# Kernel tuning notes

Measured on AMD Instinct MI355X. Metric: run time of the kernel, lower is better.

Reference implementation:

```python
import jax, jax.numpy as jnp
import numpy as np

B, T, D, H, O = 1024, 2048, 13, 128, 2


def setup_inputs() -> dict:
    key = jax.random.key(0)
    k1, k2, k3, k4 = jax.random.split(key, 4)
    xs = jax.random.normal(k1, (B, T, D), dtype=jnp.float32)
    # nn.Linear(in, out, bias=False) weights: [out, in]
    W_in = jax.random.normal(k2, (H, D), dtype=jnp.float32) / np.sqrt(D).astype(np.float32)
    W_h = jax.random.normal(k3, (H, H), dtype=jnp.float32) / np.sqrt(H).astype(np.float32)
    W_out = jax.random.normal(k4, (O, H), dtype=jnp.float32) / np.sqrt(H).astype(np.float32)
    return {"xs": xs, "W_in": W_in, "W_h": W_h, "W_out": W_out}


def reference(xs, W_in, W_h, W_out):
    # Vanilla hardtanh RNN, h0 = 0 (first step y = hardtanh(in_h(x)) == hardtanh(in_h(x) + W_h @ 0)).
    # Precompute all input projections in one big GEMM: [B, T, H]
    pre = jnp.einsum('btd,hd->bth', xs, W_in)

    def step(h, xh_t):  # h: [B, H], xh_t: [B, H]
        h = jnp.clip(xh_t + h @ W_h.T, -1.0, 1.0)  # F.hardtanh
        return h, None

    h0 = jnp.zeros((xs.shape[0], W_in.shape[0]), dtype=xs.dtype)
    hT, _ = jax.lax.scan(step, h0, jnp.swapaxes(pre, 0, 1))  # scan over time
    # Only the final hidden state per sequence is projected to the output.
    return hT @ W_out.T  # [B, O]
```

## Files before the change

### kernel.cpp

```cpp
#include <hip/hip_runtime.h>
#include <stdint.h>


#define RNN_B 1024
#define RNN_T 2048
#define RNN_D 13
#define RNN_H 128
#define RNN_O 2

#define NB 16
#define NWAVE 4
#define NTHR (NWAVE * 64)

using f32x4 = __attribute__((ext_vector_type(4))) float;
using v8s   = __attribute__((ext_vector_type(8))) short;

__device__ __forceinline__ short f2bf(float f) {
    union { float f; uint32_t u; } c; c.f = f;
    uint32_t u = c.u + 0x7fffu + ((c.u >> 16) & 1u);
    return (short)(u >> 16);
}
__device__ __forceinline__ float bf2fs(short s) {
    union { uint32_t u; float f; } c; c.u = ((uint32_t)(uint16_t)s) << 16;
    return c.f;
}
__device__ __forceinline__ float bitf(uint32_t u) {
    union { uint32_t u; float f; } c; c.u = u; return c.f;
}
__device__ __forceinline__ uint32_t cvtpk(float a, float b) {
    uint32_t r;
    asm("v_cvt_pk_bf16_f32 %0, %1, %2" : "=v"(r) : "v"(a), "v"(b));
    return r;
}
__device__ __forceinline__ v8s pack4(uint32_t a, uint32_t b, uint32_t c, uint32_t d) {
    union { uint32_t u[4]; v8s s; } z;
    z.u[0] = a; z.u[1] = b; z.u[2] = c; z.u[3] = d; return z.s;
}
__device__ __forceinline__ float clamp1(float v) {
    return __builtin_amdgcn_fmed3f(v, -1.0f, 1.0f);
}

__device__ __forceinline__ void barrier_lgkm() {
    __builtin_amdgcn_sched_barrier(0);
    asm volatile("s_waitcnt lgkmcnt(0)" ::: "memory");
    __builtin_amdgcn_s_barrier();
    asm volatile("" ::: "memory");
    __builtin_amdgcn_sched_barrier(0);
}

#define MFMA(a, b, c) __builtin_amdgcn_mfma_f32_16x16x32_bf16((a), (b), (c), 0, 0, 0)

#define STEP(CUR, NXT, X0, X1, X2, X3, TPF)                                      \
  do {                                                                           \
                     \
    v8s bh1 = *(const v8s*)&Hhi[CUR][off1];                                      \
    v8s bl1 = *(const v8s*)&Hlo[CUR][off1];                                      \
    v8s bh2 = *(const v8s*)&Hhi[CUR][off2];                                      \
    v8s bl2 = *(const v8s*)&Hlo[CUR][off2];                                      \
    v8s bh3 = *(const v8s*)&Hhi[CUR][off3];                                      \
    v8s bl3 = *(const v8s*)&Hlo[CUR][off3];                                      \
                                \
    float m0 = X0, m1 = X1, m2 = X2, m3 = X3;                                    \
    if (g == 3) { m1 = 0.0f; m2 = 0.0f; m3 = 0.0f; }                             \
    uint32_t xh01 = cvtpk(m0, m1), xh23 = cvtpk(m2, m3);                         \
    float q0 = m0 - bitf(xh01 << 16);                                            \
    float q1 = m1 - bitf(xh01 & 0xffff0000u);                                    \
    float q2 = m2 - bitf(xh23 << 16);                                            \
    float q3 = m3 - bitf(xh23 & 0xffff0000u);                                    \
    uint32_t xl01 = cvtpk(q0, q1), xl23 = cvtpk(q2, q3);                         \
    v8s xh = pack4(xh01, xh23, 0u, 0u);                                          \
    v8s xl = pack4(xl01, xl23, 0u, 0u);                                          \
                    \
    f32x4 Z = {0.f, 0.f, 0.f, 0.f};                                              \
    f32x4 A1 = MFMA(whiA[4], xh, Z);                                             \
    f32x4 A2 = MFMA(whiA[4], xl, Z);                                             \
    f32x4 A3 = MFMA(wloA[4], xh, Z);                                             \
    A1 = MFMA(whiA[0], selfBh, A1);                                              \
    A2 = MFMA(whiA[0], selfBl, A2);                                              \
    A3 = MFMA(wloA[0], selfBh, A3);                                              \
             \
    if ((TPF) < RNN_T) {                                                         \
      const float* xp = xrow + (size_t)(TPF) * RNN_D;                            \
      X0 = xp[d0]; X1 = xp[d1]; X2 = xp[d2]; X3 = xp[d3];                        \
    }                                                                            \
    A1 = MFMA(whiA[1], bh1, A1);                                                 \
    A2 = MFMA(whiA[1], bl1, A2);                                                 \
    A3 = MFMA(wloA[1], bh1, A3);                                                 \
    A1 = MFMA(whiA[2], bh2, A1);                                                 \
    A2 = MFMA(whiA[2], bl2, A2);                                                 \
    A3 = MFMA(wloA[2], bh2, A3);                                                 \
    A1 = MFMA(whiA[3], bh3, A1);                                                 \
    A2 = MFMA(whiA[3], bl3, A2);                                                 \
    A3 = MFMA(wloA[3], bh3, A3);                                                 \
                \
    f32x4 B1 = MFMA(whiB[4], xh, Z);                                             \
    f32x4 B2 = MFMA(whiB[4], xl, Z);                                             \
    f32x4 B3 = MFMA(wloB[4], xh, Z);                                             \
    B1 = MFMA(whiB[0], selfBh, B1);                                              \
    B2 = MFMA(whiB[0], selfBl, B2);                                              \
    B3 = MFMA(wloB[0], selfBh, B3);                                              \
    float v0 = clamp1(A1[0] + A2[0] + A3[0]);                                    \
    float v1 = clamp1(A1[1] + A2[1] + A3[1]);                                    \
    float v2 = clamp1(A1[2] + A2[2] + A3[2]);                                    \
    float v3 = clamp1(A1[3] + A2[3] + A3[3]);                                    \
    B1 = MFMA(whiB[1], bh1, B1);                                                 \
    B2 = MFMA(whiB[1], bl1, B2);                                                 \
    B3 = MFMA(wloB[1], bh1, B3);                                                 \
    uint32_t h01A = cvtpk(v0, v1), h23A = cvtpk(v2, v3);                         \
    float p0 = v0 - bitf(h01A << 16);                                            \
    float p1 = v1 - bitf(h01A & 0xffff0000u);                                    \
    float p2 = v2 - bitf(h23A << 16);                                            \
    float p3 = v3 - bitf(h23A & 0xffff0000u);                                    \
    B1 = MFMA(whiB[2], bh2, B1);                                                 \
    B2 = MFMA(whiB[2], bl2, B2);                                                 \
    B3 = MFMA(wloB[2], bh2, B3);                                                 \
    uint32_t l01A = cvtpk(p0, p1), l23A = cvtpk(p2, p3);                         \
    B1 = MFMA(whiB[3], bh3, B1);                                                 \
    B2 = MFMA(whiB[3], bl3, B2);                                                 \
    B3 = MFMA(wloB[3], bh3, B3);                                                 \
        \
    {                                                                            \
      float w0 = clamp1(B1[0] + B2[0] + B3[0]);                                  \
      float w1 = clamp1(B1[1] + B2[1] + B3[1]);                                  \
      float w2 = clamp1(B1[2] + B2[2] + B3[2]);                                  \
      float w3 = clamp1(B1[3] + B2[3] + B3[3]);                                  \
      uint32_t h01B = cvtpk(w0, w1), h23B = cvtpk(w2, w3);                       \
      float r0 = w0 - bitf(h01B << 16);                                          \
      float r1 = w1 - bitf(h01B & 0xffff0000u);                                  \
      float r2 = w2 - bitf(h23B << 16);                                          \
      float r3 = w3 - bitf(h23B & 0xffff0000u);                                  \
      uint32_t l01B = cvtpk(r0, r1), l23B = cvtpk(r2, r3);                       \
      selfBh = pack4(h01A, h23A, h01B, h23B);                                    \
      selfBl = pack4(l01A, l23A, l01B, l23B);                                    \
      *(v8s*)&Hhi[NXT][offw] = selfBh;                                           \
      *(v8s*)&Hlo[NXT][offw] = selfBl;                                           \
    }                                                                            \
    barrier_lgkm();                                                              \
  } while (0)

__global__ __launch_bounds__(NTHR, 1) void rnn_mfma18_kernel(
    const float* __restrict__ xs,
    const float* __restrict__ W_in,
    const float* __restrict__ W_h,
    const float* __restrict__ W_out,
    float* __restrict__ out)
{
    __shared__ __align__(16) short Hhi[2][NB * 128];
    __shared__ __align__(16) short Hlo[2][NB * 128];

    const int tid  = threadIdx.x;
    const int lane = tid & 63;
    const int wid  = tid >> 6;
    const int n    = lane & 15;
    const int g    = lane >> 4;
    const int b0   = blockIdx.x * NB;

    const int off1 = n * 128 + (((((wid + 1) & 3) << 2) + g) ^ n) * 8;
    const int off2 = n * 128 + (((((wid + 2) & 3) << 2) + g) ^ n) * 8;
    const int off3 = n * 128 + (((((wid + 3) & 3) << 2) + g) ^ n) * 8;
    const int offw = n * 128 + (((wid << 2) + g) ^ n) * 8;

    const int d0 = (4 * g + 0 > 12) ? 12 : 4 * g + 0;
    const int d1 = (4 * g + 1 > 12) ? 12 : 4 * g + 1;
    const int d2 = (4 * g + 2 > 12) ? 12 : 4 * g + 2;
    const int d3 = (4 * g + 3 > 12) ? 12 : 4 * g + 3;

    v8s whiA[5], wloA[5], whiB[5], wloB[5];
    #pragma unroll
    for (int mi = 0; mi < 2; ++mi) {
        const int row = 16 * (wid * 2 + mi) + n;
        #pragma unroll
        for (int q = 0; q < 4; ++q) {
            const int kt = (wid + q) & 3;
            v8s h8, l8;
            #pragma unroll
            for (int j = 0; j < 4; ++j) {
                const float w1 = W_h[row * RNN_H + 32 * kt + 4 * g + j];
                const float w2 = W_h[row * RNN_H + 32 * kt + 16 + 4 * g + j];
                const short h1 = f2bf(w1);
                const short h2 = f2bf(w2);
                h8[j] = h1; h8[4 + j] = h2;
                l8[j] = f2bf(w1 - bf2fs(h1));
                l8[4 + j] = f2bf(w2 - bf2fs(h2));
            }
            if (mi == 0) { whiA[q] = h8; wloA[q] = l8; }
            else         { whiB[q] = h8; wloB[q] = l8; }
        }
        {
            v8s h8, l8;
            #pragma unroll
            for (int j = 0; j < 4; ++j) {
                const int kx = 4 * g + j;
                const float w1 = (kx < RNN_D) ? W_in[row * RNN_D + kx] : 0.0f;
                const short h1 = f2bf(w1);
                h8[j] = h1; h8[4 + j] = 0;
                l8[j] = f2bf(w1 - bf2fs(h1));
                l8[4 + j] = 0;
            }
            if (mi == 0) { whiA[4] = h8; wloA[4] = l8; }
            else         { whiB[4] = h8; wloB[4] = l8; }
        }
    }

    for (int idx = tid; idx < NB * 128; idx += NTHR) {
        Hhi[0][idx] = 0;
        Hlo[0][idx] = 0;
    }

    v8s selfBh = {0, 0, 0, 0, 0, 0, 0, 0};
    v8s selfBl = {0, 0, 0, 0, 0, 0, 0, 0};

    const float* xrow = xs + (size_t)(b0 + n) * RNN_T * RNN_D;
    float xa0 = xrow[d0], xa1 = xrow[d1], xa2 = xrow[d2], xa3 = xrow[d3];
    float xb0 = xrow[RNN_D + d0], xb1 = xrow[RNN_D + d1];
    float xb2 = xrow[RNN_D + d2], xb3 = xrow[RNN_D + d3];
    __syncthreads();

    for (int t = 0; t < RNN_T; t += 2) {
        STEP(0, 1, xa0, xa1, xa2, xa3, t + 2);
        STEP(1, 0, xb0, xb1, xb2, xb3, t + 3);
    }

    __syncthreads();

    if (wid == 0 && lane < NB * RNN_O) {
        const int nn = lane & 15;
        const int o  = lane >> 4;
        float acc = 0.0f;
        for (int i = 0; i < RNN_H; ++i) {
            const int pos = 32 * (i >> 5) + 8 * ((i >> 2) & 3)
                          + 4 * ((i >> 4) & 1) + (i & 3);
            const int adr = nn * 128 + ((pos >> 3) ^ nn) * 8 + (pos & 7);
            const float hv = bf2fs(Hhi[0][adr]) + bf2fs(Hlo[0][adr]);
            acc = fmaf(W_out[o * RNN_H + i], hv, acc);
        }
        out[(size_t)(b0 + nn) * RNN_O + o] = acc;
    }
}

extern "C" void kernel_launch(void* const* d_in, const int* in_sizes, int n_in,
                              void* d_out, int out_size, void* d_ws, size_t ws_size,
                              hipStream_t stream) {
    const float* xs    = (const float*)d_in[0];
    const float* W_in  = (const float*)d_in[1];
    const float* W_h   = (const float*)d_in[2];
    const float* W_out = (const float*)d_in[3];
    float* out = (float*)d_out;

    rnn_mfma18_kernel<<<RNN_B / NB, NTHR, 0, stream>>>(xs, W_in, W_h, W_out, out);
}
```

Measured before the change: 1.217 ms.

## Ping-pong two batch groups per block to overlap MFMA phase with epilogue

Each block now handles 32 sequences as two independent 16-sequence groups of four waves, each with its own double-buffered hidden-state LDS. The recurrent step is split into an MFMA phase and a clamp/convert/store phase, and the groups run out of phase: one group does its matrix multiplies while the other does its epilogue, separated by block barriers. The MFMA chains for the two output tiles are also interleaved, so independent accumulators hide MFMA latency. The cost is twice as many barriers per time step, shared across 8 waves, and half as many blocks.

```diff
diff --git a/kernel.cpp b/kernel.cpp
--- a/kernel.cpp
+++ b/kernel.cpp
@@ -8,9 +8,10 @@
 #define RNN_H 128
 #define RNN_O 2
 
-#define NB 16
-#define NWAVE 4
-#define NTHR (NWAVE * 64)
+#define NBPG 16
+#define NB   32
+#define NBLK (RNN_B / NB)
+#define NTHR 512
 
 using f32x4 = __attribute__((ext_vector_type(4))) float;
 using v8s   = __attribute__((ext_vector_type(8))) short;
@@ -50,16 +51,14 @@
 
 #define MFMA(a, b, c) __builtin_amdgcn_mfma_f32_16x16x32_bf16((a), (b), (c), 0, 0, 0)
 
-#define STEP(CUR, NXT, X0, X1, X2, X3, TPF)                                      \
+#define S1(BUFR, X0, X1, X2, X3, TPF)                                            \
   do {                                                                           \
-                     \
-    v8s bh1 = *(const v8s*)&Hhi[CUR][off1];                                      \
-    v8s bl1 = *(const v8s*)&Hlo[CUR][off1];                                      \
-    v8s bh2 = *(const v8s*)&Hhi[CUR][off2];                                      \
-    v8s bl2 = *(const v8s*)&Hlo[CUR][off2];                                      \
-    v8s bh3 = *(const v8s*)&Hhi[CUR][off3];                                      \
-    v8s bl3 = *(const v8s*)&Hlo[CUR][off3];                                      \
-                                \
+    v8s bh1 = *(const v8s*)&Hh[BUFR][off1];                                      \
+    v8s bl1 = *(const v8s*)&Hl[BUFR][off1];                                      \
+    v8s bh2 = *(const v8s*)&Hh[BUFR][off2];                                      \
+    v8s bl2 = *(const v8s*)&Hl[BUFR][off2];                                      \
+    v8s bh3 = *(const v8s*)&Hh[BUFR][off3];                                      \
+    v8s bl3 = *(const v8s*)&Hl[BUFR][off3];                                      \
     float m0 = X0, m1 = X1, m2 = X2, m3 = X3;                                    \
     if (g == 3) { m1 = 0.0f; m2 = 0.0f; m3 = 0.0f; }                             \
     uint32_t xh01 = cvtpk(m0, m1), xh23 = cvtpk(m2, m3);                         \
@@ -70,95 +69,97 @@
     uint32_t xl01 = cvtpk(q0, q1), xl23 = cvtpk(q2, q3);                         \
     v8s xh = pack4(xh01, xh23, 0u, 0u);                                          \
     v8s xl = pack4(xl01, xl23, 0u, 0u);                                          \
-                    \
     f32x4 Z = {0.f, 0.f, 0.f, 0.f};                                              \
-    f32x4 A1 = MFMA(whiA[4], xh, Z);                                             \
-    f32x4 A2 = MFMA(whiA[4], xl, Z);                                             \
-    f32x4 A3 = MFMA(wloA[4], xh, Z);                                             \
-    A1 = MFMA(whiA[0], selfBh, A1);                                              \
-    A2 = MFMA(whiA[0], selfBl, A2);                                              \
-    A3 = MFMA(wloA[0], selfBh, A3);                                              \
-             \
+    P1 = MFMA(whiA[4], xh, Z);                                                   \
+    Q1 = MFMA(whiB[4], xh, Z);                                                   \
+    P2 = MFMA(whiA[4], xl, Z);                                                   \
+    Q2 = MFMA(whiB[4], xl, Z);                                                   \
+    P3 = MFMA(wloA[4], xh, Z);                                                   \
+    Q3 = MFMA(wloB[4], xh, Z);                                                   \
+    P1 = MFMA(whiA[0], selfBh, P1);                                              \
+    Q1 = MFMA(whiB[0], selfBh, Q1);                                              \
+    P2 = MFMA(whiA[0], selfBl, P2);                                              \
+    Q2 = MFMA(whiB[0], selfBl, Q2);                                              \
+    P3 = MFMA(wloA[0], selfBh, P3);                                              \
+    Q3 = MFMA(wloB[0], selfBh, Q3);                                              \
     if ((TPF) < RNN_T) {                                                         \
       const float* xp = xrow + (size_t)(TPF) * RNN_D;                            \
       X0 = xp[d0]; X1 = xp[d1]; X2 = xp[d2]; X3 = xp[d3];                        \
     }                                                                            \
-    A1 = MFMA(whiA[1], bh1, A1);                                                 \
-    A2 = MFMA(whiA[1], bl1, A2);                                                 \
-    A3 = MFMA(wloA[1], bh1, A3);                                                 \
-    A1 = MFMA(whiA[2], bh2, A1);                                                 \
-    A2 = MFMA(whiA[2], bl2, A2);                                                 \
-    A3 = MFMA(wloA[2], bh2, A3);                                                 \
-    A1 = MFMA(whiA[3], bh3, A1);                                                 \
-    A2 = MFMA(whiA[3], bl3, A2);                                                 \
-    A3 = MFMA(wloA[3], bh3, A3);                                                 \
-                \
-    f32x4 B1 = MFMA(whiB[4], xh, Z);                                             \
-    f32x4 B2 = MFMA(whiB[4], xl, Z);                                             \
-    f32x4 B3 = MFMA(wloB[4], xh, Z);                                             \
-    B1 = MFMA(whiB[0], selfBh, B1);                                              \
-    B2 = MFMA(whiB[0], selfBl, B2);                                              \
-    B3 = MFMA(wloB[0], selfBh, B3);                                              \
-    float v0 = clamp1(A1[0] + A2[0] + A3[0]);                                    \
-    float v1 = clamp1(A1[1] + A2[1] + A3[1]);                                    \
-    float v2 = clamp1(A1[2] + A2[2] + A3[2]);                                    \
-    float v3 = clamp1(A1[3] + A2[3] + A3[3]);                                    \
-    B1 = MFMA(whiB[1], bh1, B1);                                                 \
-    B2 = MFMA(whiB[1], bl1, B2);                                                 \
-    B3 = MFMA(wloB[1], bh1, B3);                                                 \
+    P1 = MFMA(whiA[1], bh1, P1);                                                 \
+    Q1 = MFMA(whiB[1], bh1, Q1);                                                 \
+    P2 = MFMA(whiA[1], bl1, P2);                                                 \
+    Q2 = MFMA(whiB[1], bl1, Q2);                                                 \
+    P3 = MFMA(wloA[1], bh1, P3);                                                 \
+    Q3 = MFMA(wloB[1], bh1, Q3);                                                 \
+    P1 = MFMA(whiA[2], bh2, P1);                                                 \
+    Q1 = MFMA(whiB[2], bh2, Q1);                                                 \
+    P2 = MFMA(whiA[2], bl2, P2);                                                 \
+    Q2 = MFMA(whiB[2], bl2, Q2);                                                 \
+    P3 = MFMA(wloA[2], bh2, P3);                                                 \
+    Q3 = MFMA(wloB[2], bh2, Q3);                                                 \
+    P1 = MFMA(whiA[3], bh3, P1);                                                 \
+    Q1 = MFMA(whiB[3], bh3, Q1);                                                 \
+    P2 = MFMA(whiA[3], bl3, P2);                                                 \
+    Q2 = MFMA(whiB[3], bl3, Q2);                                                 \
+    P3 = MFMA(wloA[3], bh3, P3);                                                 \
+    Q3 = MFMA(wloB[3], bh3, Q3);                                                 \
+  } while (0)
+
+#define S2(BUFW)                                                                 \
+  do {                                                                           \
+    float v0 = clamp1(P1[0] + P2[0] + P3[0]);                                    \
+    float v1 = clamp1(P1[1] + P2[1] + P3[1]);                                    \
+    float v2 = clamp1(P1[2] + P2[2] + P3[2]);                                    \
+    float v3 = clamp1(P1[3] + P2[3] + P3[3]);                                    \
     uint32_t h01A = cvtpk(v0, v1), h23A = cvtpk(v2, v3);                         \
     float p0 = v0 - bitf(h01A << 16);                                            \
     float p1 = v1 - bitf(h01A & 0xffff0000u);                                    \
     float p2 = v2 - bitf(h23A << 16);                                            \
     float p3 = v3 - bitf(h23A & 0xffff0000u);                                    \
-    B1 = MFMA(whiB[2], bh2, B1);                                                 \
-    B2 = MFMA(whiB[2], bl2, B2);                                                 \
-    B3 = MFMA(wloB[2], bh2, B3);                                                 \
     uint32_t l01A = cvtpk(p0, p1), l23A = cvtpk(p2, p3);                         \
-    B1 = MFMA(whiB[3], bh3, B1);                                                 \
-    B2 = MFMA(whiB[3], bl3, B2);                                                 \
-    B3 = MFMA(wloB[3], bh3, B3);                                                 \
-        \
-    {                                                                            \
-      float w0 = clamp1(B1[0] + B2[0] + B3[0]);                                  \
-      float w1 = clamp1(B1[1] + B2[1] + B3[1]);                                  \
-      float w2 = clamp1(B1[2] + B2[2] + B3[2]);                                  \
-      float w3 = clamp1(B1[3] + B2[3] + B3[3]);                                  \
-      uint32_t h01B = cvtpk(w0, w1), h23B = cvtpk(w2, w3);                       \
-      float r0 = w0 - bitf(h01B << 16);                                          \
-      float r1 = w1 - bitf(h01B & 0xffff0000u);                                  \
-      float r2 = w2 - bitf(h23B << 16);                                          \
-      float r3 = w3 - bitf(h23B & 0xffff0000u);                                  \
-      uint32_t l01B = cvtpk(r0, r1), l23B = cvtpk(r2, r3);                       \
-      selfBh = pack4(h01A, h23A, h01B, h23B);                                    \
-      selfBl = pack4(l01A, l23A, l01B, l23B);                                    \
-      *(v8s*)&Hhi[NXT][offw] = selfBh;                                           \
-      *(v8s*)&Hlo[NXT][offw] = selfBl;                                           \
-    }                                                                            \
-    barrier_lgkm();                                                              \
+    float w0 = clamp1(Q1[0] + Q2[0] + Q3[0]);                                    \
+    float w1 = clamp1(Q1[1] + Q2[1] + Q3[1]);                                    \
+    float w2 = clamp1(Q1[2] + Q2[2] + Q3[2]);                                    \
+    float w3 = clamp1(Q1[3] + Q2[3] + Q3[3]);                                    \
+    uint32_t h01B = cvtpk(w0, w1), h23B = cvtpk(w2, w3);                         \
+    float r0 = w0 - bitf(h01B << 16);                                            \
+    float r1 = w1 - bitf(h01B & 0xffff0000u);                                    \
+    float r2 = w2 - bitf(h23B << 16);                                            \
+    float r3 = w3 - bitf(h23B & 0xffff0000u);                                    \
+    uint32_t l01B = cvtpk(r0, r1), l23B = cvtpk(r2, r3);                         \
+    selfBh = pack4(h01A, h23A, h01B, h23B);                                      \
+    selfBl = pack4(l01A, l23A, l01B, l23B);                                      \
+    *(v8s*)&Hh[BUFW][offw] = selfBh;                                             \
+    *(v8s*)&Hl[BUFW][offw] = selfBl;                                             \
   } while (0)
 
-__global__ __launch_bounds__(NTHR, 1) void rnn_mfma18_kernel(
+__global__ __launch_bounds__(NTHR, 1) void rnn_mfma20_kernel(
     const float* __restrict__ xs,
     const float* __restrict__ W_in,
     const float* __restrict__ W_h,
     const float* __restrict__ W_out,
     float* __restrict__ out)
 {
-    __shared__ __align__(16) short Hhi[2][NB * 128];
-    __shared__ __align__(16) short Hlo[2][NB * 128];
+    __shared__ __align__(16) short Hhi[2][2][NBPG * 128];
+    __shared__ __align__(16) short Hlo[2][2][NBPG * 128];
 
     const int tid  = threadIdx.x;
     const int lane = tid & 63;
     const int wid  = tid >> 6;
+    const int grp  = __builtin_amdgcn_readfirstlane(wid >> 2);
+    const int wg   = wid & 3;
     const int n    = lane & 15;
     const int g    = lane >> 4;
-    const int b0   = blockIdx.x * NB;
-
-    const int off1 = n * 128 + (((((wid + 1) & 3) << 2) + g) ^ n) * 8;
-    const int off2 = n * 128 + (((((wid + 2) & 3) << 2) + g) ^ n) * 8;
-    const int off3 = n * 128 + (((((wid + 3) & 3) << 2) + g) ^ n) * 8;
-    const int offw = n * 128 + (((wid << 2) + g) ^ n) * 8;
+    const int b0   = blockIdx.x * NB + grp * NBPG;
+
+    short (*Hh)[NBPG * 128] = Hhi[grp];
+    short (*Hl)[NBPG * 128] = Hlo[grp];
+
+    const int off1 = n * 128 + (((((wg + 1) & 3) << 2) + g) ^ n) * 8;
+    const int off2 = n * 128 + (((((wg + 2) & 3) << 2) + g) ^ n) * 8;
+    const int off3 = n * 128 + (((((wg + 3) & 3) << 2) + g) ^ n) * 8;
+    const int offw = n * 128 + (((wg << 2) + g) ^ n) * 8;
 
     const int d0 = (4 * g + 0 > 12) ? 12 : 4 * g + 0;
     const int d1 = (4 * g + 1 > 12) ? 12 : 4 * g + 1;
@@ -168,10 +169,10 @@
     v8s whiA[5], wloA[5], whiB[5], wloB[5];
     #pragma unroll
     for (int mi = 0; mi < 2; ++mi) {
-        const int row = 16 * (wid * 2 + mi) + n;
+        const int row = 16 * (wg * 2 + mi) + n;
         #pragma unroll
         for (int q = 0; q < 4; ++q) {
-            const int kt = (wid + q) & 3;
+            const int kt = (wg + q) & 3;
             v8s h8, l8;
             #pragma unroll
             for (int j = 0; j < 4; ++j) {
@@ -202,13 +203,15 @@
         }
     }
 
-    for (int idx = tid; idx < NB * 128; idx += NTHR) {
-        Hhi[0][idx] = 0;
-        Hlo[0][idx] = 0;
+    for (int idx = tid; idx < 2 * 2 * NBPG * 128; idx += NTHR) {
+        (&Hhi[0][0][0])[idx] = 0;
+        (&Hlo[0][0][0])[idx] = 0;
     }
 
     v8s selfBh = {0, 0, 0, 0, 0, 0, 0, 0};
     v8s selfBl = {0, 0, 0, 0, 0, 0, 0, 0};
+    f32x4 P1 = {0.f, 0.f, 0.f, 0.f};
+    f32x4 P2 = P1, P3 = P1, Q1 = P1, Q2 = P1, Q3 = P1;
 
     const float* xrow = xs + (size_t)(b0 + n) * RNN_T * RNN_D;
     float xa0 = xrow[d0], xa1 = xrow[d1], xa2 = xrow[d2], xa3 = xrow[d3];
@@ -216,14 +219,25 @@
     float xb2 = xrow[RNN_D + d2], xb3 = xrow[RNN_D + d3];
     __syncthreads();
 
-    for (int t = 0; t < RNN_T; t += 2) {
-        STEP(0, 1, xa0, xa1, xa2, xa3, t + 2);
-        STEP(1, 0, xb0, xb1, xb2, xb3, t + 3);
-    }
-
+    for (int k = 0; k < RNN_T / 2; ++k) {
+        const int t2 = 2 * k;
+        if (grp == 0) { S1(0, xa0, xa1, xa2, xa3, t2 + 2); }
+        else if (k)   { S2(0); }
+        barrier_lgkm();
+        if (grp == 0) { S2(1); }
+        else          { S1(0, xa0, xa1, xa2, xa3, t2 + 2); }
+        barrier_lgkm();
+        if (grp == 0) { S1(1, xb0, xb1, xb2, xb3, t2 + 3); }
+        else          { S2(1); }
+        barrier_lgkm();
+        if (grp == 0) { S2(0); }
+        else          { S1(1, xb0, xb1, xb2, xb3, t2 + 3); }
+        barrier_lgkm();
+    }
+    if (grp == 1) { S2(0); }
     __syncthreads();
 
-    if (wid == 0 && lane < NB * RNN_O) {
+    if (wg == 0 && lane < NBPG * RNN_O) {
         const int nn = lane & 15;
         const int o  = lane >> 4;
         float acc = 0.0f;
@@ -231,7 +245,7 @@
             const int pos = 32 * (i >> 5) + 8 * ((i >> 2) & 3)
                           + 4 * ((i >> 4) & 1) + (i & 3);
             const int adr = nn * 128 + ((pos >> 3) ^ nn) * 8 + (pos & 7);
-            const float hv = bf2fs(Hhi[0][adr]) + bf2fs(Hlo[0][adr]);
+            const float hv = bf2fs(Hh[0][adr]) + bf2fs(Hl[0][adr]);
             acc = fmaf(W_out[o * RNN_H + i], hv, acc);
         }
         out[(size_t)(b0 + nn) * RNN_O + o] = acc;
@@ -247,5 +261,5 @@
     const float* W_out = (const float*)d_in[3];
     float* out = (float*)d_out;
 
-    rnn_mfma18_kernel<<<RNN_B / NB, NTHR, 0, stream>>>(xs, W_in, W_h, W_out, out);
-}
+    rnn_mfma20_kernel<<<NBLK, NTHR, 0, stream>>>(xs, W_in, W_h, W_out, out);
+}
```

After: 2.995 ms. 2.46x slower.

## Software-pipeline next step's input and self-block MFMAs across the barrier

Applied to the files above, without the earlier changes.

Each step now issues the next timestep's input-projection MFMAs and its own-block recurrent MFMAs (which need only this wave's freshly computed hidden slice) after the LDS store and before the barrier. This takes those MFMAs off the critical path that follows the barrier. The A and B accumulator chains are also interleaved so two independent MFMA chains hide each other's latency. The cost is more live accumulator registers held across the barrier and a prologue that seeds the first step.

```diff
diff --git a/kernel.cpp b/kernel.cpp
--- a/kernel.cpp
+++ b/kernel.cpp
@@ -50,95 +50,107 @@
 
 #define MFMA(a, b, c) __builtin_amdgcn_mfma_f32_16x16x32_bf16((a), (b), (c), 0, 0, 0)
 
-#define STEP(CUR, NXT, X0, X1, X2, X3, TPF)                                      \
+#define XCONV(XH, XL, C0, C1, C2, C3)                                            \
   do {                                                                           \
-                     \
+    float cm0 = C0, cm1 = C1, cm2 = C2, cm3 = C3;                                \
+    if (g == 3) { cm1 = 0.0f; cm2 = 0.0f; cm3 = 0.0f; }                          \
+    uint32_t ch01 = cvtpk(cm0, cm1), ch23 = cvtpk(cm2, cm3);                     \
+    float cq0 = cm0 - bitf(ch01 << 16);                                          \
+    float cq1 = cm1 - bitf(ch01 & 0xffff0000u);                                  \
+    float cq2 = cm2 - bitf(ch23 << 16);                                          \
+    float cq3 = cm3 - bitf(ch23 & 0xffff0000u);                                  \
+    uint32_t cl01 = cvtpk(cq0, cq1), cl23 = cvtpk(cq2, cq3);                     \
+    XH = pack4(ch01, ch23, 0u, 0u);                                              \
+    XL = pack4(cl01, cl23, 0u, 0u);                                              \
+  } while (0)
+
+#define SEED(XH, XL)                                                             \
+  do {                                                                           \
+    f32x4 Z = {0.f, 0.f, 0.f, 0.f};                                              \
+    A1 = MFMA(whiA[4], XH, Z);                                                   \
+    B1 = MFMA(whiB[4], XH, Z);                                                   \
+    A2 = MFMA(whiA[4], XL, Z);                                                   \
+    B2 = MFMA(whiB[4], XL, Z);                                                   \
+    A3 = MFMA(wloA[4], XH, Z);                                                   \
+    B3 = MFMA(wloB[4], XH, Z);                                                   \
+    A1 = MFMA(whiA[0], selfBh, A1);                                              \
+    B1 = MFMA(whiB[0], selfBh, B1);                                              \
+    A2 = MFMA(whiA[0], selfBl, A2);                                              \
+    B2 = MFMA(whiB[0], selfBl, B2);                                              \
+    A3 = MFMA(wloA[0], selfBh, A3);                                              \
+    B3 = MFMA(wloB[0], selfBh, B3);                                              \
+  } while (0)
+
+#define STEPP(CUR, NXT, C0, C1, C2, C3, P0, P1, P2, P3, TPF)                     \
+  do {                                                                           \
+                                   \
     v8s bh1 = *(const v8s*)&Hhi[CUR][off1];                                      \
     v8s bl1 = *(const v8s*)&Hlo[CUR][off1];                                      \
     v8s bh2 = *(const v8s*)&Hhi[CUR][off2];                                      \
     v8s bl2 = *(const v8s*)&Hlo[CUR][off2];                                      \
     v8s bh3 = *(const v8s*)&Hhi[CUR][off3];                                      \
     v8s bl3 = *(const v8s*)&Hlo[CUR][off3];                                      \
+                             \
+    v8s xhn, xln;                                                                \
+    XCONV(xhn, xln, C0, C1, C2, C3);                                             \
                                 \
-    float m0 = X0, m1 = X1, m2 = X2, m3 = X3;                                    \
-    if (g == 3) { m1 = 0.0f; m2 = 0.0f; m3 = 0.0f; }                             \
-    uint32_t xh01 = cvtpk(m0, m1), xh23 = cvtpk(m2, m3);                         \
-    float q0 = m0 - bitf(xh01 << 16);                                            \
-    float q1 = m1 - bitf(xh01 & 0xffff0000u);                                    \
-    float q2 = m2 - bitf(xh23 << 16);                                            \
-    float q3 = m3 - bitf(xh23 & 0xffff0000u);                                    \
-    uint32_t xl01 = cvtpk(q0, q1), xl23 = cvtpk(q2, q3);                         \
-    v8s xh = pack4(xh01, xh23, 0u, 0u);                                          \
-    v8s xl = pack4(xl01, xl23, 0u, 0u);                                          \
-                    \
-    f32x4 Z = {0.f, 0.f, 0.f, 0.f};                                              \
-    f32x4 A1 = MFMA(whiA[4], xh, Z);                                             \
-    f32x4 A2 = MFMA(whiA[4], xl, Z);                                             \
-    f32x4 A3 = MFMA(wloA[4], xh, Z);                                             \
-    A1 = MFMA(whiA[0], selfBh, A1);                                              \
-    A2 = MFMA(whiA[0], selfBl, A2);                                              \
-    A3 = MFMA(wloA[0], selfBh, A3);                                              \
-             \
-    if ((TPF) < RNN_T) {                                                         \
-      const float* xp = xrow + (size_t)(TPF) * RNN_D;                            \
-      X0 = xp[d0]; X1 = xp[d1]; X2 = xp[d2]; X3 = xp[d3];                        \
-    }                                                                            \
     A1 = MFMA(whiA[1], bh1, A1);                                                 \
+    B1 = MFMA(whiB[1], bh1, B1);                                                 \
     A2 = MFMA(whiA[1], bl1, A2);                                                 \
+    B2 = MFMA(whiB[1], bl1, B2);                                                 \
     A3 = MFMA(wloA[1], bh1, A3);                                                 \
+    B3 = MFMA(wloB[1], bh1, B3);                                                 \
     A1 = MFMA(whiA[2], bh2, A1);                                                 \
+    B1 = MFMA(whiB[2], bh2, B1);                                                 \
     A2 = MFMA(whiA[2], bl2, A2);                                                 \
+    B2 = MFMA(whiB[2], bl2, B2);                                                 \
     A3 = MFMA(wloA[2], bh2, A3);                                                 \
+    B3 = MFMA(wloB[2], bh2, B3);                                                 \
     A1 = MFMA(whiA[3], bh3, A1);                                                 \
+    B1 = MFMA(whiB[3], bh3, B1);                                                 \
     A2 = MFMA(whiA[3], bl3, A2);                                                 \
+    B2 = MFMA(whiB[3], bl3, B2);                                                 \
     A3 = MFMA(wloA[3], bh3, A3);                                                 \
-                \
-    f32x4 B1 = MFMA(whiB[4], xh, Z);                                             \
-    f32x4 B2 = MFMA(whiB[4], xl, Z);                                             \
-    f32x4 B3 = MFMA(wloB[4], xh, Z);                                             \
-    B1 = MFMA(whiB[0], selfBh, B1);                                              \
-    B2 = MFMA(whiB[0], selfBl, B2);                                              \
-    B3 = MFMA(wloB[0], selfBh, B3);                                              \
+    B3 = MFMA(wloB[3], bh3, B3);                                                 \
+                                                              \
     float v0 = clamp1(A1[0] + A2[0] + A3[0]);                                    \
     float v1 = clamp1(A1[1] + A2[1] + A3[1]);                                    \
     float v2 = clamp1(A1[2] + A2[2] + A3[2]);                                    \
     float v3 = clamp1(A1[3] + A2[3] + A3[3]);                                    \
-    B1 = MFMA(whiB[1], bh1, B1);                                                 \
-    B2 = MFMA(whiB[1], bl1, B2);                                                 \
-    B3 = MFMA(wloB[1], bh1, B3);                                                 \
     uint32_t h01A = cvtpk(v0, v1), h23A = cvtpk(v2, v3);                         \
     float p0 = v0 - bitf(h01A << 16);                                            \
     float p1 = v1 - bitf(h01A & 0xffff0000u);                                    \
     float p2 = v2 - bitf(h23A << 16);                                            \
     float p3 = v3 - bitf(h23A & 0xffff0000u);                                    \
-    B1 = MFMA(whiB[2], bh2, B1);                                                 \
-    B2 = MFMA(whiB[2], bl2, B2);                                                 \
-    B3 = MFMA(wloB[2], bh2, B3);                                                 \
     uint32_t l01A = cvtpk(p0, p1), l23A = cvtpk(p2, p3);                         \
-    B1 = MFMA(whiB[3], bh3, B1);                                                 \
-    B2 = MFMA(whiB[3], bl3, B2);                                                 \
-    B3 = MFMA(wloB[3], bh3, B3);                                                 \
-        \
-    {                                                                            \
-      float w0 = clamp1(B1[0] + B2[0] + B3[0]);                                  \
-      float w1 = clamp1(B1[1] + B2[1] + B3[1]);                                  \
-      float w2 = clamp1(B1[2] + B2[2] + B3[2]);                                  \
-      float w3 = clamp1(B1[3] + B2[3] + B3[3]);                                  \
-      uint32_t h01B = cvtpk(w0, w1), h23B = cvtpk(w2, w3);                       \
-      float r0 = w0 - bitf(h01B << 16);                                          \
-      float r1 = w1 - bitf(h01B & 0xffff0000u);                                  \
-      float r2 = w2 - bitf(h23B << 16);                                          \
-      float r3 = w3 - bitf(h23B & 0xffff0000u);                                  \
-      uint32_t l01B = cvtpk(r0, r1), l23B = cvtpk(r2, r3);                       \
-      selfBh = pack4(h01A, h23A, h01B, h23B);                                    \
-      selfBl = pack4(l01A, l23A, l01B, l23B);                                    \
-      *(v8s*)&Hhi[NXT][offw] = selfBh;                                           \
-      *(v8s*)&Hlo[NXT][offw] = selfBl;                                           \
+                                   \
+    float w0 = clamp1(B1[0] + B2[0] + B3[0]);                                    \
+    float w1 = clamp1(B1[1] + B2[1] + B3[1]);                                    \
+    float w2 = clamp1(B1[2] + B2[2] + B3[2]);                                    \
+    float w3 = clamp1(B1[3] + B2[3] + B3[3]);                                    \
+    uint32_t h01B = cvtpk(w0, w1), h23B = cvtpk(w2, w3);                         \
+    float r0 = w0 - bitf(h01B << 16);                                            \
+    float r1 = w1 - bitf(h01B & 0xffff0000u);                                    \
+    float r2 = w2 - bitf(h23B << 16);                                            \
+    float r3 = w3 - bitf(h23B & 0xffff0000u);                                    \
+    uint32_t l01B = cvtpk(r0, r1), l23B = cvtpk(r2, r3);                         \
+    selfBh = pack4(h01A, h23A, h01B, h23B);                                      \
+    selfBl = pack4(l01A, l23A, l01B, l23B);                                      \
+                  \
+    *(v8s*)&Hhi[NXT][offw] = selfBh;                                             \
+    *(v8s*)&Hlo[NXT][offw] = selfBl;                                             \
+         \
+    SEED(xhn, xln);                                                              \
+                   \
+    if ((TPF) < RNN_T) {                                                         \
+      const float* xp = xrow + (size_t)(TPF) * RNN_D;                            \
+      P0 = xp[d0]; P1 = xp[d1]; P2 = xp[d2]; P3 = xp[d3];                        \
     }                                                                            \
+                                                              \
     barrier_lgkm();                                                              \
   } while (0)
 
-__global__ __launch_bounds__(NTHR, 1) void rnn_mfma18_kernel(
+__global__ __launch_bounds__(NTHR, 1) void rnn_mfma21_kernel(
     const float* __restrict__ xs,
     const float* __restrict__ W_in,
     const float* __restrict__ W_h,
@@ -214,11 +226,18 @@
     float xa0 = xrow[d0], xa1 = xrow[d1], xa2 = xrow[d2], xa3 = xrow[d3];
     float xb0 = xrow[RNN_D + d0], xb1 = xrow[RNN_D + d1];
     float xb2 = xrow[RNN_D + d2], xb3 = xrow[RNN_D + d3];
+
+    f32x4 A1, A2, A3, B1, B2, B3;
+    {
+        v8s xh0, xl0;
+        XCONV(xh0, xl0, xa0, xa1, xa2, xa3);
+        SEED(xh0, xl0);
+    }
     __syncthreads();
 
     for (int t = 0; t < RNN_T; t += 2) {
-        STEP(0, 1, xa0, xa1, xa2, xa3, t + 2);
-        STEP(1, 0, xb0, xb1, xb2, xb3, t + 3);
+        STEPP(0, 1, xb0, xb1, xb2, xb3, xa0, xa1, xa2, xa3, t + 2);
+        STEPP(1, 0, xa0, xa1, xa2, xa3, xb0, xb1, xb2, xb3, t + 3);
     }
 
     __syncthreads();
@@ -247,5 +266,5 @@
     const float* W_out = (const float*)d_in[3];
     float* out = (float*)d_out;
 
-    rnn_mfma18_kernel<<<RNN_B / NB, NTHR, 0, stream>>>(xs, W_in, W_h, W_out, out);
-}
+    rnn_mfma21_kernel<<<RNN_B / NB, NTHR, 0, stream>>>(xs, W_in, W_h, W_out, out);
+}
```

Result: slower. 1.376 ms (+13.0%).
